# Performance work log

Measured on AMD Instinct MI355X. Metric: run time of the kernel, lower is better.

## Reference

```python
import jax, jax.numpy as jnp
import numpy as np
from jax import lax

SIGMA = 1
KSIZE = SIGMA * 4 + 1  # 5-tap, odd -> torch 'same' == lax 'SAME'


def _gauss1d():
    half = (KSIZE - 1) * 0.5
    x = np.linspace(-half, half, KSIZE)
    pdf = np.exp(-0.5 * (x / SIGMA) ** 2)
    return jnp.asarray(pdf / pdf.sum(), dtype=jnp.float32)


def _blur(x):
    # separable depthwise 3D gaussian blur: three sequential 1D convs (D, H, W)
    k = _gauss1d().astype(x.dtype)
    C = x.shape[1]
    dn = lax.conv_dimension_numbers(x.shape, (C, 1, KSIZE, 1, 1), ('NCDHW', 'OIDHW', 'NCDHW'))
    for ax in range(3):
        kshape = [1, 1, 1]
        kshape[ax] = KSIZE
        w = jnp.broadcast_to(k.reshape(kshape)[None, None], (C, 1, *kshape))
        x = lax.conv_general_dilated(x, w, (1, 1, 1), 'SAME',
                                     dimension_numbers=dn, feature_group_count=C)
    return x


def setup_inputs() -> dict:
    key = jax.random.key(0)
    kA, kB, kM = jax.random.split(key, 3)
    shape = (2, 1, 160, 192, 224)
    return {
        'image_A': jax.random.normal(kA, shape, dtype=jnp.float32),
        'image_B': jax.random.normal(kB, shape, dtype=jnp.float32),
        'mask_A': jax.random.uniform(kM, shape, dtype=jnp.float32),
    }


def reference(image_A, image_B, mask_A):
    I, J = image_A, image_B
    bI = _blur(I)
    bJ = _blur(J)
    cross = _blur(I * J) - bI * bJ
    varI = jax.nn.relu(_blur(I * I) - bI ** 2) + 1e-05
    varJ = jax.nn.relu(_blur(J * J) - bJ ** 2) + 1e-05
    lncc = 1.0 - cross / jnp.sqrt(varI * varJ)
    return jnp.sum(lncc * mask_A) / (jnp.sum(mask_A) + 1e-08)
```

## Files before the change

### kernel.cpp

```cpp
#include <hip/hip_runtime.h>


#define NB 2
#define DD 160
#define HH 192
#define WW 224
#define SH 224
#define SD (224*192)
#define SN (224*192*160)

#define TW 32
#define TH 16
#define ROWS (TH+4)
#define DCHUNK 32
#define NCHUNK (DD/DCHUNK)

#define K0 0.05448868f
#define K1 0.24420134f
#define K2 0.40261995f

typedef float v2f __attribute__((ext_vector_type(2)));
typedef float v4f __attribute__((ext_vector_type(4)));

__global__ __launch_bounds__(640) void lncc_main(
    const float* __restrict__ A, const float* __restrict__ B,
    const float* __restrict__ M, double* __restrict__ acc)
{
    __shared__ v2f  sIJ[2][ROWS][36];
    __shared__ v4f  wbA[2][ROWS][32];
    __shared__ float wbC[2][ROWS][32];
    __shared__ float redL[10], redM[10];

    const int wt = blockIdx.x;
    const int ht = blockIdx.y;
    const int zz = blockIdx.z;
    const int n  = (zz >= NCHUNK) ? 1 : 0;
    const int dc = zz - n * NCHUNK;
    const int w0 = wt * TW, h0 = ht * TH, d0 = dc * DCHUNK;

    const float* __restrict__ Ai = A + (size_t)n * SN;
    const float* __restrict__ Bi = B + (size_t)n * SN;
    const float* __restrict__ Mi = M + (size_t)n * SN;

    const int tid = threadIdx.x;
    const int r   = tid >> 5;
    const int c   = tid & 31;

    const int gh  = h0 + r - 2;
    const bool hv = (unsigned)gh < (unsigned)HH;
    const int ghc = hv ? gh : 0;
    const int hwm = ghc * SH + (w0 + c);
    const int gwl = w0 + c - 2, gwr = w0 + c + 2;
    const bool lv = hv && (c < 2)   && (gwl >= 0);
    const bool rv = hv && (c >= 30) && (gwr < WW);
    const bool anyh = lv || rv;
    const int hwh = ghc * SH + (lv ? gwl : (rv ? gwr : 0));
    const int mbase = (h0 + r) * SH + (w0 + c);
    const bool orow = (r < TH);

    v2f pP0 = 0.f, pP1 = 0.f, pP2 = 0.f, pP3 = 0.f;
    v2f pQ0 = 0.f, pQ1 = 0.f, pQ2 = 0.f, pQ3 = 0.f;
    float pC0 = 0.f, pC1 = 0.f, pC2 = 0.f, pC3 = 0.f;
    float accL = 0.f, accM = 0.f;

    v2f nM = 0.f, nH = 0.f;

    auto stage = [&](int pw) {
        sIJ[pw][r][c + 2] = nM;
        if (c < 2)        sIJ[pw][r][c]     = nH;
        else if (c >= 30) sIJ[pw][r][c + 4] = nH;
    };
    auto prefetch = [&](int dd, bool guard) {
        nM = 0.f; nH = 0.f;
        if (guard) {
            const int dof = dd * SD;
            if (hv)   { nM.x = Ai[dof + hwm]; nM.y = Bi[dof + hwm]; }
            if (anyh) { nH.x = Ai[dof + hwh]; nH.y = Bi[dof + hwh]; }
        }
    };
    auto wblur = [&](int px) {
        const v2f v0 = sIJ[px][r][c];
        const v2f v1 = sIJ[px][r][c + 1];
        const v2f v2 = sIJ[px][r][c + 2];
        const v2f v3 = sIJ[px][r][c + 3];
        const v2f v4 = sIJ[px][r][c + 4];
        const v2f b  = K0*(v0+v4) + K1*(v1+v3) + K2*v2;
        const v2f bs = K0*(v0*v0+v4*v4) + K1*(v1*v1+v3*v3) + K2*(v2*v2);
        const float bij = K0*(v0.x*v0.y+v4.x*v4.y) + K1*(v1.x*v1.y+v3.x*v3.y) + K2*(v2.x*v2.y);
        wbA[px][r][c] = (v4f){b.x, b.y, bs.x, bs.y};
        wbC[px][r][c] = bij;
    };
    auto hblur = [&](int pw, float mval, bool doout) {
        const v4f a0 = wbA[pw][r][c];
        const v4f a1 = wbA[pw][r + 1][c];
        const v4f a2 = wbA[pw][r + 2][c];
        const v4f a3 = wbA[pw][r + 3][c];
        const v4f a4 = wbA[pw][r + 4][c];
        const float c0 = wbC[pw][r][c];
        const float c1 = wbC[pw][r + 1][c];
        const float c2 = wbC[pw][r + 2][c];
        const float c3 = wbC[pw][r + 3][c];
        const float c4 = wbC[pw][r + 4][c];
        const v2f h1 = K0*(a0.xy+a4.xy) + K1*(a1.xy+a3.xy) + K2*a2.xy;
        const v2f h2 = K0*(a0.zw+a4.zw) + K1*(a1.zw+a3.zw) + K2*a2.zw;
        const float hc = K0*(c0+c4) + K1*(c1+c3) + K2*c2;

        if (doout) {
            const v2f bP = K0*(pP0+h1) + K1*(pP1+pP3) + K2*pP2;
            const v2f bS = K0*(pQ0+h2) + K1*(pQ1+pQ3) + K2*pQ2;
            const float bC = K0*(pC0+hc) + K1*(pC1+pC3) + K2*pC2;
            const float cross = bC - bP.x * bP.y;
            const float vI = fmaxf(bS.x - bP.x * bP.x, 0.f) + 1e-5f;
            const float vJ = fmaxf(bS.y - bP.y * bP.y, 0.f) + 1e-5f;
            const float lncc = 1.0f - cross * rsqrtf(vI * vJ);
            accL += lncc * mval;
            accM += mval;
        }

        pP0 = pP1; pP1 = pP2; pP2 = pP3; pP3 = h1;
        pQ0 = pQ1; pQ1 = pQ2; pQ2 = pQ3; pQ3 = h2;
        pC0 = pC1; pC1 = pC2; pC2 = pC3; pC3 = hc;
    };

    {
        const int dd = d0 - 2;
        prefetch(dd, dd >= 0);
    }

    for (int k = 0; k < 6; ++k) {
        const int pw = k & 1, px = pw ^ 1;
        stage(pw);
        const int dd = d0 - 1 + k;
        prefetch(dd, dd >= 0);
        if (k >= 1) wblur(px);
        if (k >= 2 && orow) hblur(pw, 0.f, false);
        __syncthreads();
    }

#pragma unroll 2
    for (int k = 6; k < DCHUNK + 3; ++k) {
        const int pw = k & 1, px = pw ^ 1;
        stage(pw);
        const int dd = d0 - 1 + k;
        prefetch(dd, dd < DD);
        float mval = 0.f;
        if (orow) mval = Mi[(d0 - 6 + k) * SD + mbase];
        wblur(px);
        if (orow) hblur(pw, mval, true);
        __syncthreads();
    }

    {
        stage(1);
        float mval = 0.f;
        if (orow) mval = Mi[(d0 + DCHUNK - 3) * SD + mbase];
        wblur(0);
        if (orow) hblur(1, mval, true);
        __syncthreads();
    }
    {
        float mval = 0.f;
        if (orow) mval = Mi[(d0 + DCHUNK - 2) * SD + mbase];
        wblur(1);
        if (orow) hblur(0, mval, true);
        __syncthreads();
    }
    {
        float mval = 0.f;
        if (orow) {
            mval = Mi[(d0 + DCHUNK - 1) * SD + mbase];
            hblur(1, mval, true);
        }
    }

#pragma unroll
    for (int off = 32; off > 0; off >>= 1) {
        accL += __shfl_down(accL, off, 64);
        accM += __shfl_down(accM, off, 64);
    }
    const int wave = tid >> 6;
    if ((tid & 63) == 0) { redL[wave] = accL; redM[wave] = accM; }
    __syncthreads();
    if (tid == 0) {
        float sL = 0.f, sM = 0.f;
#pragma unroll
        for (int kk = 0; kk < 10; ++kk) { sL += redL[kk]; sM += redM[kk]; }
        atomicAdd(&acc[0], (double)sL);
        atomicAdd(&acc[1], (double)sM);
    }
}

__global__ void lncc_final(const double* __restrict__ acc, float* __restrict__ out)
{
    out[0] = (float)(acc[0] / (acc[1] + 1e-8));
}

extern "C" void kernel_launch(void* const* d_in, const int* in_sizes, int n_in,
                              void* d_out, int out_size, void* d_ws, size_t ws_size,
                              hipStream_t stream)
{
    const float* A = (const float*)d_in[0];
    const float* B = (const float*)d_in[1];
    const float* M = (const float*)d_in[2];
    double* acc = (double*)d_ws;

    hipMemsetAsync(d_ws, 0, 2 * sizeof(double), stream);

    dim3 grid(WW / TW, HH / TH, NB * NCHUNK);
    dim3 block(640);
    hipLaunchKernelGGL(lncc_main, grid, block, 0, stream, A, B, M, acc);
    hipLaunchKernelGGL(lncc_final, dim3(1), dim3(1), 0, stream, acc, (float*)d_out);
}
```

Measured before the change: 255.4 us.

## Shrink depth chunks, prefetch mask ahead, use LDS-only barrier

```diff
diff --git a/kernel.cpp b/kernel.cpp
--- a/kernel.cpp
+++ b/kernel.cpp
@@ -12,12 +12,14 @@
 #define TW 32
 #define TH 16
 #define ROWS (TH+4)
-#define DCHUNK 32
+#define DCHUNK 20
 #define NCHUNK (DD/DCHUNK)
 
 #define K0 0.05448868f
 #define K1 0.24420134f
 #define K2 0.40261995f
+
+#define BAR() asm volatile("s_waitcnt lgkmcnt(0)\n\ts_barrier" ::: "memory")
 
 typedef float v2f __attribute__((ext_vector_type(2)));
 typedef float v4f __attribute__((ext_vector_type(4)));
@@ -34,8 +36,8 @@
     const int wt = blockIdx.x;
     const int ht = blockIdx.y;
     const int zz = blockIdx.z;
-    const int n  = (zz >= NCHUNK) ? 1 : 0;
-    const int dc = zz - n * NCHUNK;
+    const int n  = zz >> 3;
+    const int dc = zz & 7;
     const int w0 = wt * TW, h0 = ht * TH, d0 = dc * DCHUNK;
 
     const float* __restrict__ Ai = A + (size_t)n * SN;
@@ -64,13 +66,14 @@
     float accL = 0.f, accM = 0.f;
 
     v2f nM = 0.f, nH = 0.f;
+    float mvN = 0.f;
 
     auto stage = [&](int pw) {
         sIJ[pw][r][c + 2] = nM;
         if (c < 2)        sIJ[pw][r][c]     = nH;
         else if (c >= 30) sIJ[pw][r][c + 4] = nH;
     };
-    auto prefetch = [&](int dd, bool guard) {
+    auto pref = [&](int dd, bool guard) {
         nM = 0.f; nH = 0.f;
         if (guard) {
             const int dof = dd * SD;
@@ -124,53 +127,51 @@
 
     {
         const int dd = d0 - 2;
-        prefetch(dd, dd >= 0);
+        pref(dd, dd >= 0);
     }
 
     for (int k = 0; k < 6; ++k) {
         const int pw = k & 1, px = pw ^ 1;
         stage(pw);
         const int dd = d0 - 1 + k;
-        prefetch(dd, dd >= 0);
+        pref(dd, dd >= 0);
+        if (k == 5 && orow) mvN = Mi[d0 * SD + mbase];
         if (k >= 1) wblur(px);
         if (k >= 2 && orow) hblur(pw, 0.f, false);
-        __syncthreads();
-    }
-
+        BAR();
+    }
+
+    int moff = (d0 + 1) * SD + mbase;
 #pragma unroll 2
-    for (int k = 6; k < DCHUNK + 3; ++k) {
+    for (int k = 6; k < 23; ++k) {
         const int pw = k & 1, px = pw ^ 1;
         stage(pw);
         const int dd = d0 - 1 + k;
-        prefetch(dd, dd < DD);
-        float mval = 0.f;
-        if (orow) mval = Mi[(d0 - 6 + k) * SD + mbase];
+        pref(dd, dd < DD);
+        const float mval = mvN;
+        if (orow) { mvN = Mi[moff]; moff += SD; }
         wblur(px);
         if (orow) hblur(pw, mval, true);
-        __syncthreads();
+        BAR();
     }
 
     {
         stage(1);
-        float mval = 0.f;
-        if (orow) mval = Mi[(d0 + DCHUNK - 3) * SD + mbase];
+        const float mval = mvN;
+        if (orow) mvN = Mi[moff];
         wblur(0);
         if (orow) hblur(1, mval, true);
-        __syncthreads();
-    }
-    {
-        float mval = 0.f;
-        if (orow) mval = Mi[(d0 + DCHUNK - 2) * SD + mbase];
+        BAR();
+    }
+    {
+        const float mval = mvN;
+        if (orow) mvN = Mi[(d0 + 19) * SD + mbase];
         wblur(1);
         if (orow) hblur(0, mval, true);
-        __syncthreads();
-    }
-    {
-        float mval = 0.f;
-        if (orow) {
-            mval = Mi[(d0 + DCHUNK - 1) * SD + mbase];
-            hblur(1, mval, true);
-        }
+        BAR();
+    }
+    {
+        if (orow) hblur(1, mvN, true);
     }
 
 #pragma unroll
```

Result: faster. 227.7 us (-10.8%).
